# Kernel tuning notes

Measured on AMD Instinct MI355X. Metric: run time of the kernel, lower is better.

The kernel has to match this reference:

```python
import jax, jax.numpy as jnp
import numpy as np

B, S, D_MODEL = 2, 8192, 768
NUM_HEADS = 12
R = 4          # dilation_rate (= number of independent attention branches)
SEG = 512      # segment_size


def setup_inputs() -> dict:
    key = jax.random.key(0)
    ks = jax.random.split(key, 3)
    x = jax.random.normal(ks[0], (B, S, D_MODEL), jnp.float32)
    # Per-offset MHA weights: fused qkv proj and output proj (bias zeros)
    Wqkv = jax.random.normal(ks[1], (R, 3 * D_MODEL, D_MODEL), jnp.float32) * 0.02
    bqkv = jnp.zeros((R, 3 * D_MODEL), jnp.float32)
    Wout = jax.random.normal(ks[2], (R, D_MODEL, D_MODEL), jnp.float32) * 0.02
    bout = jnp.zeros((R, D_MODEL), jnp.float32)
    return {"x": x, "Wqkv": Wqkv, "bqkv": bqkv, "Wout": Wout, "bout": bout,
            "num_heads": NUM_HEADS}


def reference(x, Wqkv, bqkv, Wout, bout, num_heads):
    Bb, Ss, D = x.shape
    r = Wqkv.shape[0]
    L = Ss // r                # tokens per dilation offset
    n_seg = L // SEG           # segments per offset
    hd = D // num_heads

    # Dilated strided gather: x[:, o::r, :] for all offsets o -> (r, B, L, D)
    xo = jnp.moveaxis(x.reshape(Bb, L, r, D), 2, 0)

    # Per-offset fused qkv projection
    qkv = jnp.einsum('rbld,red->rble', xo, Wqkv) + bqkv[:, None, None, :]
    q, k, v = jnp.split(qkv, 3, axis=-1)
    seg = lambda t: t.reshape(r, Bb, n_seg, SEG, num_heads, hd)
    q, k, v = seg(q), seg(k), seg(v)  # (r, B, n_seg, SEG, H, hd)

    scale = 1.0 / np.sqrt(hd).astype(np.float32)
    scores = jnp.einsum('rbnqhd,rbnkhd->rbnhqk', q, k) * scale
    attn = jax.nn.softmax(scores, axis=-1)
    ctx = jnp.einsum('rbnhqk,rbnkhd->rbnqhd', attn, v).reshape(r, Bb, L, D)

    # Per-offset output projection
    out = jnp.einsum('rbld,red->rble', ctx, Wout) + bout[:, None, None, :]  # (r,B,L,D)

    # Scatter each offset's output back to its strided positions, zeros elsewhere,
    # then concat over offsets along the feature dim -> (B, S, r*D)
    res = jnp.zeros((Bb, Ss, r * D), x.dtype)
    for o in range(r):  # fixed small loop over dilation offsets
        res = res.at[:, o::r, o * D:(o + 1) * D].set(out[o])
    return res
```

## Files before the change

### kernel.cpp

```cpp
#include <hip/hip_runtime.h>

constexpr int Bb   = 2;
constexpr int S    = 8192;
constexpr int D    = 768;
constexpr int H    = 12;
constexpr int HD   = 64;
constexpr int R    = 4;
constexpr int L    = 2048;
constexpr int SEG  = 512;
constexpr int NSEG = 4;
constexpr int E3   = 3 * D;
constexpr int RD   = R * D;

typedef _Float16 f16x8 __attribute__((ext_vector_type(8)));
typedef _Float16 f16x4 __attribute__((ext_vector_type(4)));
typedef float    f32x4 __attribute__((ext_vector_type(4)));

#define AS1 __attribute__((address_space(1)))
#define AS3 __attribute__((address_space(3)))

__device__ __forceinline__ void gld16(const void* g, void* l) {
    __builtin_amdgcn_global_load_lds((AS1 void*)g, (AS3 void*)l, 16, 0, 0);
}

__global__ __launch_bounds__(256) void conv_one(const float4* __restrict__ x,
                                                f16x4* __restrict__ o, int n4)
{
    int i = blockIdx.x * 256 + threadIdx.x;
    const int stride = gridDim.x * 256;
    for (; i < n4; i += stride) {
        float4 v = x[i];
        f16x4 h;
        h[0] = (_Float16)v.x; h[1] = (_Float16)v.y;
        h[2] = (_Float16)v.z; h[3] = (_Float16)v.w;
        o[i] = h;
    }
}

template <int MODE>
__global__ __launch_bounds__(256) void mfma_gemm(const _Float16* __restrict__ Ah0,
                                                 const _Float16* __restrict__ Wh0,
                                                 const float* __restrict__ B0,
                                                 _Float16* __restrict__ Q0,
                                                 _Float16* __restrict__ K0,
                                                 _Float16* __restrict__ V0,
                                                 float* __restrict__ C0)
{
    constexpr int NXB = (MODE == 0) ? 18 : 6;
    constexpr int NWG = NXB * 16 * 8;
    const int wg = ((int)blockIdx.x & 7) * (NWG >> 3) + ((int)blockIdx.x >> 3);
    const int n0 = (wg % NXB) * 128;
    const int m0 = ((wg / NXB) & 15) * 128;
    const int z  = wg / (NXB * 16);
    const int r = z >> 1, b = z & 1;

    const _Float16* Ah; const _Float16* Wh; const float* bias;
    int lda;
    if (MODE == 0) {
        Ah = Ah0 + ((size_t)b * S + r) * D;  lda = RD;
        Wh = Wh0 + (size_t)r * E3 * D;
        bias = B0 + r * E3;
    } else {
        Ah = Ah0 + (size_t)z * L * D;        lda = D;
        Wh = Wh0 + (size_t)r * D * D;
        bias = B0 + r * D;
    }

    const int tid  = threadIdx.x;
    const int wave = tid >> 6;
    const int lane = tid & 63;
    const int lw   = lane & 15;
    const int quad = lane >> 4;
    const int wm   = wave & 1, wn = wave >> 1;

    __shared__ _Float16 sm[3][2][4096];

    f32x4 acc[4][4];
    #pragma unroll
    for (int mt = 0; mt < 4; mt++)
        #pragma unroll
        for (int nt = 0; nt < 4; nt++)
            acc[mt][nt] = f32x4{0.f, 0.f, 0.f, 0.f};

    const int srow = lane & 15;
    const int scol = (lane >> 4) * 8;

    auto stage = [&](int buf, int k0) {
        #pragma unroll
        for (int i = 0; i < 4; i++) {
            const int idx  = wave * 4 + i;
            const int tile = idx >> 3, g = idx & 7;
            const _Float16* src = (tile == 0) ? Ah : Wh;
            const int ldr   = (tile == 0) ? lda : D;
            const int base0 = (tile == 0) ? m0 : n0;
            gld16(src + (size_t)(base0 + g * 16 + srow) * ldr + k0 + scol,
                  &sm[buf][tile][g * 512]);
        }
    };

    stage(0, 0);
    stage(1, 32);

    for (int k = 0; k < 24; k++) {
        asm volatile("s_waitcnt lgkmcnt(0)" ::: "memory");
        if (k == 23) asm volatile("s_waitcnt vmcnt(0)" ::: "memory");
        else         asm volatile("s_waitcnt vmcnt(4)" ::: "memory");
        __builtin_amdgcn_s_barrier();
        __builtin_amdgcn_sched_barrier(0);

        const int buf = k % 3;
        f16x8 af[4], bf[4];
        #pragma unroll
        for (int mt = 0; mt < 4; mt++)
            af[mt] = *(const f16x8*)&sm[buf][0][(wm * 4 + mt) * 512 + quad * 128 + lw * 8];
        #pragma unroll
        for (int nt = 0; nt < 4; nt++)
            bf[nt] = *(const f16x8*)&sm[buf][1][(wn * 4 + nt) * 512 + quad * 128 + lw * 8];
        if (k + 2 < 24) stage((k + 2) % 3, (k + 2) * 32);
        #pragma unroll
        for (int mt = 0; mt < 4; mt++)
            #pragma unroll
            for (int nt = 0; nt < 4; nt++)
                acc[mt][nt] = __builtin_amdgcn_mfma_f32_16x16x32_f16(af[mt], bf[nt], acc[mt][nt], 0, 0, 0);
    }
    __syncthreads();

    float bv[4];
    #pragma unroll
    for (int nt = 0; nt < 4; nt++)
        bv[nt] = bias[n0 + wn * 64 + nt * 16 + lw];

    if (MODE == 0) {
        const int reg = n0 / D;
        if (reg < 2) {
            _Float16* G = (reg == 0 ? Q0 : K0) + (size_t)z * L * D;
            const int colbase = (n0 - reg * D) + wn * 64;
            _Float16* wbuf = &sm[0][0][wave * 2048];
            #pragma unroll
            for (int p = 0; p < 2; p++) {
                #pragma unroll
                for (int mtl = 0; mtl < 2; mtl++) {
                    const int mt = p * 2 + mtl;
                    #pragma unroll
                    for (int nt = 0; nt < 4; nt++)
                        #pragma unroll
                        for (int rr = 0; rr < 4; rr++)
                            wbuf[(mtl * 16 + quad * 4 + rr) * 64 + nt * 16 + lw] =
                                (_Float16)(acc[mt][nt][rr] + bv[nt]);
                }
                asm volatile("s_waitcnt lgkmcnt(0)" ::: "memory");
                #pragma unroll
                for (int j = 0; j < 4; j++) {
                    const int rl = (lane >> 3) + j * 8;
                    f16x8 v = *(const f16x8*)&wbuf[rl * 64 + (lane & 7) * 8];
                    const int l = m0 + wm * 64 + p * 32 + rl;
                    *(f16x8*)(G + (size_t)l * D + colbase + (lane & 7) * 8) = v;
                }
                asm volatile("s_waitcnt lgkmcnt(0)" ::: "memory");
            }
        } else {
            #pragma unroll
            for (int nt = 0; nt < 4; nt++) {
                const int e  = (n0 - 2 * D) + wn * 64 + nt * 16 + lw;
                const int hh = e >> 6, hd = e & 63;
                #pragma unroll
                for (int mt = 0; mt < 4; mt++) {
                    const int l = m0 + wm * 64 + mt * 16 + quad * 4;
                    const int ns = l >> 9, key = l & 511;
                    f16x4 v;
                    #pragma unroll
                    for (int rr = 0; rr < 4; rr++)
                        v[rr] = (_Float16)(acc[mt][nt][rr] + bv[nt]);
                    *(f16x4*)(V0 + ((size_t)((z * H + hh) * NSEG + ns)) * (HD * SEG)
                              + (size_t)hd * SEG + key) = v;
                }
            }
        }
    } else {
        float* Crow = C0 + (size_t)b * S * RD;
        #pragma unroll
        for (int mt = 0; mt < 4; mt++)
            #pragma unroll
            for (int nt = 0; nt < 4; nt++) {
                const int col = n0 + wn * 64 + nt * 16 + lw;
                #pragma unroll
                for (int rr = 0; rr < 4; rr++) {
                    const int l = m0 + wm * 64 + mt * 16 + quad * 4 + rr;
                    const float val = acc[mt][nt][rr] + bv[nt];
                    const size_t rowoff = (size_t)(l * R + r) * RD;
                    #pragma unroll
                    for (int rp = 0; rp < 4; rp++)
                        Crow[rowoff + rp * D + col] = (rp == r) ? val : 0.f;
                }
            }
    }
}

__global__ __launch_bounds__(256) void attn_mfma(const _Float16* __restrict__ Qh,
                                                 const _Float16* __restrict__ Kh,
                                                 const _Float16* __restrict__ Vt,
                                                 _Float16* __restrict__ ctx)
{
    __shared__ _Float16 Ks[3][4096];
    __shared__ _Float16 Vs[3][4096];
    __shared__ _Float16 Pw[16384];

    int t = ((int)blockIdx.x & 7) * 96 + ((int)blockIdx.x >> 3);
    const int qh = t & 1; t >>= 1;
    const int h  = t % H; t /= H;
    const int n  = t & 3; t >>= 2;
    const int z  = t;

    const int tid  = threadIdx.x;
    const int wave = tid >> 6;
    const int lane = tid & 63;
    const int lw   = lane & 15;
    const int quad = lane >> 4;
    const int srow = lane & 15;
    const int scol = (lane >> 4) * 8;

    const _Float16* Qg = Qh + ((size_t)(z * L + n * SEG + qh * 256)) * D + h * HD;
    #pragma unroll
    for (int i = 0; i < 8; i++) {
        const int qg = wave * 4 + (i >> 1), h2 = i & 1;
        gld16(Qg + (size_t)(qg * 16 + srow) * D + h2 * 32 + scol,
              &Pw[qg * 1024 + h2 * 512]);
    }
    __syncthreads();

    f16x8 qf[4][2];
    #pragma unroll
    for (int mt = 0; mt < 4; mt++)
        #pragma unroll
        for (int kk = 0; kk < 2; kk++)
            qf[mt][kk] = *(const f16x8*)&Pw[(wave * 4 + mt) * 1024 + (kk * 4 + quad) * 128 + lw * 8];

    const _Float16* Kg = Kh + ((size_t)(z * L + n * SEG)) * D + h * HD;
    const _Float16* Vg = Vt + ((size_t)((z * H + h) * NSEG + n)) * (HD * SEG);
    _Float16* Pv = Pw + wave * 4096;

    auto stageKV = [&](int buf, int kt) {
        #pragma unroll
        for (int i = 0; i < 4; i++) {
            const int idx = wave * 4 + i;
            const int j = idx & 7, g = j >> 1, h2 = j & 1;
            if (idx < 8)
                gld16(Kg + (size_t)(kt * 64 + g * 16 + srow) * D + h2 * 32 + scol,
                      &Ks[buf][g * 1024 + h2 * 512]);
            else
                gld16(Vg + (size_t)(g * 16 + srow) * SEG + kt * 64 + h2 * 32 + scol,
                      &Vs[buf][g * 1024 + h2 * 512]);
        }
    };

    f32x4 cacc[4][4];
    #pragma unroll
    for (int mt = 0; mt < 4; mt++)
        #pragma unroll
        for (int nt = 0; nt < 4; nt++)
            cacc[mt][nt] = f32x4{0.f, 0.f, 0.f, 0.f};
    float psum[4] = {0.f, 0.f, 0.f, 0.f};

    stageKV(0, 0);
    stageKV(1, 1);

    for (int kt = 0; kt < 8; kt++) {
        asm volatile("s_waitcnt lgkmcnt(0)" ::: "memory");
        if (kt == 7) asm volatile("s_waitcnt vmcnt(0)" ::: "memory");
        else         asm volatile("s_waitcnt vmcnt(4)" ::: "memory");
        __builtin_amdgcn_s_barrier();
        __builtin_amdgcn_sched_barrier(0);

        const int buf = kt % 3;
        if (kt + 2 < 8) stageKV((kt + 2) % 3, kt + 2);

        f32x4 Sc[4][4];
        #pragma unroll
        for (int mt = 0; mt < 4; mt++)
            #pragma unroll
            for (int nt = 0; nt < 4; nt++)
                Sc[mt][nt] = f32x4{0.f, 0.f, 0.f, 0.f};
        #pragma unroll
        for (int kk = 0; kk < 2; kk++)
            #pragma unroll
            for (int nt = 0; nt < 4; nt++) {
                f16x8 kf = *(const f16x8*)&Ks[buf][nt * 1024 + (kk * 4 + quad) * 128 + lw * 8];
                #pragma unroll
                for (int mt = 0; mt < 4; mt++)
                    Sc[mt][nt] = __builtin_amdgcn_mfma_f32_16x16x32_f16(kf, qf[mt][kk], Sc[mt][nt], 0, 0, 0);
            }

        #pragma unroll
        for (int mt = 0; mt < 4; mt++)
            #pragma unroll
            for (int nt = 0; nt < 4; nt++) {
                f16x4 p4;
                #pragma unroll
                for (int rr = 0; rr < 4; rr++)
                    p4[rr] = (_Float16)__expf(Sc[mt][nt][rr] * 0.125f);
                *(f16x4*)&Pv[mt * 1024 + (nt * 2 + (quad >> 1)) * 128 + lw * 8 + (quad & 1) * 4] = p4;
            }
        asm volatile("s_waitcnt lgkmcnt(0)" ::: "memory");

        #pragma unroll
        for (int kk = 0; kk < 2; kk++) {
            f16x8 pf[4], vf[4];
            #pragma unroll
            for (int mt = 0; mt < 4; mt++) {
                pf[mt] = *(const f16x8*)&Pv[mt * 1024 + (kk * 4 + quad) * 128 + lw * 8];
                float s = 0.f;
                #pragma unroll
                for (int j = 0; j < 8; j++) s += (float)pf[mt][j];
                psum[mt] += s;
            }
            #pragma unroll
            for (int nt = 0; nt < 4; nt++)
                vf[nt] = *(const f16x8*)&Vs[buf][nt * 1024 + (kk * 4 + quad) * 128 + lw * 8];
            #pragma unroll
            for (int mt = 0; mt < 4; mt++)
                #pragma unroll
                for (int nt = 0; nt < 4; nt++)
                    cacc[mt][nt] = __builtin_amdgcn_mfma_f32_16x16x32_f16(pf[mt], vf[nt], cacc[mt][nt], 0, 0, 0);
        }
    }

    #pragma unroll
    for (int mt = 0; mt < 4; mt++) {
        psum[mt] += __shfl_xor(psum[mt], 16);
        psum[mt] += __shfl_xor(psum[mt], 32);
    }
    _Float16* Cg = ctx + ((size_t)(z * L + n * SEG + qh * 256 + wave * 64)) * D + h * HD;
    #pragma unroll
    for (int mt = 0; mt < 4; mt++)
        #pragma unroll
        for (int rr = 0; rr < 4; rr++) {
            float iv = 1.0f / __shfl(psum[mt], quad * 4 + rr);
            int q = mt * 16 + quad * 4 + rr;
            #pragma unroll
            for (int nt = 0; nt < 4; nt++)
                Cg[(size_t)q * D + nt * 16 + lw] = (_Float16)(cacc[mt][nt][rr] * iv);
        }
}

extern "C" void kernel_launch(void* const* d_in, const int* in_sizes, int n_in,
                              void* d_out, int out_size, void* d_ws, size_t ws_size,
                              hipStream_t stream)
{
    const float* x    = (const float*)d_in[0];
    const float* Wqkv = (const float*)d_in[1];
    const float* bqkv = (const float*)d_in[2];
    const float* Wout = (const float*)d_in[3];
    const float* bout = (const float*)d_in[4];

    float* out = (float*)d_out;

    constexpr size_t NX   = (size_t)Bb * S * D;
    constexpr size_t NWQ  = (size_t)R * E3 * D;
    constexpr size_t NWO  = (size_t)R * D * D;
    constexpr size_t NTOK = (size_t)R * Bb * L;

    _Float16* Xh  = (_Float16*)d_ws;
    _Float16* Wqh = Xh  + NX;
    _Float16* Wo  = Wqh + NWQ;
    _Float16* Qh  = Wo  + NWO;
    _Float16* Kh  = Qh  + NTOK * D;
    _Float16* Vt  = Kh  + NTOK * D;
    _Float16* ctx = Vt  + NTOK * D;

    conv_one<<<2048, 256, 0, stream>>>((const float4*)x, (f16x4*)Xh, (int)(NX / 4));
    conv_one<<<2048, 256, 0, stream>>>((const float4*)Wqkv, (f16x4*)Wqh, (int)(NWQ / 4));
    conv_one<<<1024, 256, 0, stream>>>((const float4*)Wout, (f16x4*)Wo, (int)(NWO / 4));

    mfma_gemm<0><<<E3 / 128 * (L / 128) * R * Bb, 256, 0, stream>>>(
        Xh, Wqh, bqkv, Qh, Kh, Vt, nullptr);

    attn_mfma<<<R * Bb * NSEG * H * 2, 256, 0, stream>>>(Qh, Kh, Vt, ctx);

    mfma_gemm<1><<<D / 128 * (L / 128) * R * Bb, 256, 0, stream>>>(
        ctx, Wo, bout, nullptr, nullptr, nullptr, out);
}
```

Baseline: 465.6 us.

## Enlarge GEMM tiles to 256x128, fold softmax scale into Q, use MFMA row sums

Both projection GEMMs now use 512-thread blocks computing 256x128 output tiles, with eight waves arranged 4x2, so each staged weight tile is reused across twice as many rows. The softmax scale times log2(e) is folded into Q at the QKV epilogue, so attention can call exp2f directly without a multiply. Per-row softmax denominators are now accumulated by an MFMA against a ones vector, replacing the scalar fp16 summation and the cross-lane shuffles. Risks are lower occupancy from larger blocks, extra MFMA work for the sums, and fp16 precision loss from pre-scaling Q.

```diff
diff --git a/kernel.cpp b/kernel.cpp
--- a/kernel.cpp
+++ b/kernel.cpp
@@ -38,7 +38,7 @@
 }
 
 template <int MODE>
-__global__ __launch_bounds__(256) void mfma_gemm(const _Float16* __restrict__ Ah0,
+__global__ __launch_bounds__(512) void mfma_gemm(const _Float16* __restrict__ Ah0,
                                                  const _Float16* __restrict__ Wh0,
                                                  const float* __restrict__ B0,
                                                  _Float16* __restrict__ Q0,
@@ -47,11 +47,12 @@
                                                  float* __restrict__ C0)
 {
     constexpr int NXB = (MODE == 0) ? 18 : 6;
-    constexpr int NWG = NXB * 16 * 8;
+    constexpr int MB  = 8;
+    constexpr int NWG = NXB * MB * 8;
     const int wg = ((int)blockIdx.x & 7) * (NWG >> 3) + ((int)blockIdx.x >> 3);
     const int n0 = (wg % NXB) * 128;
-    const int m0 = ((wg / NXB) & 15) * 128;
-    const int z  = wg / (NXB * 16);
+    const int m0 = ((wg / NXB) & (MB - 1)) * 256;
+    const int z  = wg / (NXB * MB);
     const int r = z >> 1, b = z & 1;
 
     const _Float16* Ah; const _Float16* Wh; const float* bias;
@@ -71,9 +72,9 @@
     const int lane = tid & 63;
     const int lw   = lane & 15;
     const int quad = lane >> 4;
-    const int wm   = wave & 1, wn = wave >> 1;
-
-    __shared__ _Float16 sm[3][2][4096];
+    const int wm   = wave & 3, wn = wave >> 2;
+
+    __shared__ _Float16 sm[3][12288];
 
     f32x4 acc[4][4];
     #pragma unroll
@@ -87,14 +88,15 @@
 
     auto stage = [&](int buf, int k0) {
         #pragma unroll
-        for (int i = 0; i < 4; i++) {
-            const int idx  = wave * 4 + i;
-            const int tile = idx >> 3, g = idx & 7;
-            const _Float16* src = (tile == 0) ? Ah : Wh;
-            const int ldr   = (tile == 0) ? lda : D;
-            const int base0 = (tile == 0) ? m0 : n0;
+        for (int i = 0; i < 3; i++) {
+            const int idx  = wave * 3 + i;
+            const bool isA = idx < 16;
+            const int g    = isA ? idx : idx - 16;
+            const _Float16* src = isA ? Ah : Wh;
+            const int ldr   = isA ? lda : D;
+            const int base0 = isA ? m0 : n0;
             gld16(src + (size_t)(base0 + g * 16 + srow) * ldr + k0 + scol,
-                  &sm[buf][tile][g * 512]);
+                  &sm[buf][(isA ? 0 : 8192) + g * 512]);
         }
     };
 
@@ -104,7 +106,7 @@
     for (int k = 0; k < 24; k++) {
         asm volatile("s_waitcnt lgkmcnt(0)" ::: "memory");
         if (k == 23) asm volatile("s_waitcnt vmcnt(0)" ::: "memory");
-        else         asm volatile("s_waitcnt vmcnt(4)" ::: "memory");
+        else         asm volatile("s_waitcnt vmcnt(3)" ::: "memory");
         __builtin_amdgcn_s_barrier();
         __builtin_amdgcn_sched_barrier(0);
 
@@ -112,10 +114,10 @@
         f16x8 af[4], bf[4];
         #pragma unroll
         for (int mt = 0; mt < 4; mt++)
-            af[mt] = *(const f16x8*)&sm[buf][0][(wm * 4 + mt) * 512 + quad * 128 + lw * 8];
+            af[mt] = *(const f16x8*)&sm[buf][(wm * 4 + mt) * 512 + quad * 128 + lw * 8];
         #pragma unroll
         for (int nt = 0; nt < 4; nt++)
-            bf[nt] = *(const f16x8*)&sm[buf][1][(wn * 4 + nt) * 512 + quad * 128 + lw * 8];
+            bf[nt] = *(const f16x8*)&sm[buf][8192 + (wn * 4 + nt) * 512 + quad * 128 + lw * 8];
         if (k + 2 < 24) stage((k + 2) % 3, (k + 2) * 32);
         #pragma unroll
         for (int mt = 0; mt < 4; mt++)
@@ -133,9 +135,10 @@
     if (MODE == 0) {
         const int reg = n0 / D;
         if (reg < 2) {
+            const float qs = (reg == 0) ? 0.18033688011112042f : 1.0f;
             _Float16* G = (reg == 0 ? Q0 : K0) + (size_t)z * L * D;
             const int colbase = (n0 - reg * D) + wn * 64;
-            _Float16* wbuf = &sm[0][0][wave * 2048];
+            _Float16* wbuf = &sm[0][wave * 2048];
             #pragma unroll
             for (int p = 0; p < 2; p++) {
                 #pragma unroll
@@ -146,7 +149,7 @@
                         #pragma unroll
                         for (int rr = 0; rr < 4; rr++)
                             wbuf[(mtl * 16 + quad * 4 + rr) * 64 + nt * 16 + lw] =
-                                (_Float16)(acc[mt][nt][rr] + bv[nt]);
+                                (_Float16)((acc[mt][nt][rr] + bv[nt]) * qs);
                 }
                 asm volatile("s_waitcnt lgkmcnt(0)" ::: "memory");
                 #pragma unroll
@@ -259,7 +262,13 @@
         #pragma unroll
         for (int nt = 0; nt < 4; nt++)
             cacc[mt][nt] = f32x4{0.f, 0.f, 0.f, 0.f};
-    float psum[4] = {0.f, 0.f, 0.f, 0.f};
+    f32x4 Ps[4];
+    #pragma unroll
+    for (int mt = 0; mt < 4; mt++)
+        Ps[mt] = f32x4{0.f, 0.f, 0.f, 0.f};
+    f16x8 ones;
+    #pragma unroll
+    for (int j = 0; j < 8; j++) ones[j] = (_Float16)1.0f;
 
     stageKV(0, 0);
     stageKV(1, 1);
@@ -297,7 +306,7 @@
                 f16x4 p4;
                 #pragma unroll
                 for (int rr = 0; rr < 4; rr++)
-                    p4[rr] = (_Float16)__expf(Sc[mt][nt][rr] * 0.125f);
+                    p4[rr] = (_Float16)exp2f(Sc[mt][nt][rr]);
                 *(f16x4*)&Pv[mt * 1024 + (nt * 2 + (quad >> 1)) * 128 + lw * 8 + (quad & 1) * 4] = p4;
             }
         asm volatile("s_waitcnt lgkmcnt(0)" ::: "memory");
@@ -306,35 +315,27 @@
         for (int kk = 0; kk < 2; kk++) {
             f16x8 pf[4], vf[4];
             #pragma unroll
-            for (int mt = 0; mt < 4; mt++) {
+            for (int mt = 0; mt < 4; mt++)
                 pf[mt] = *(const f16x8*)&Pv[mt * 1024 + (kk * 4 + quad) * 128 + lw * 8];
-                float s = 0.f;
-                #pragma unroll
-                for (int j = 0; j < 8; j++) s += (float)pf[mt][j];
-                psum[mt] += s;
-            }
             #pragma unroll
             for (int nt = 0; nt < 4; nt++)
                 vf[nt] = *(const f16x8*)&Vs[buf][nt * 1024 + (kk * 4 + quad) * 128 + lw * 8];
             #pragma unroll
-            for (int mt = 0; mt < 4; mt++)
+            for (int mt = 0; mt < 4; mt++) {
+                Ps[mt] = __builtin_amdgcn_mfma_f32_16x16x32_f16(pf[mt], ones, Ps[mt], 0, 0, 0);
                 #pragma unroll
                 for (int nt = 0; nt < 4; nt++)
                     cacc[mt][nt] = __builtin_amdgcn_mfma_f32_16x16x32_f16(pf[mt], vf[nt], cacc[mt][nt], 0, 0, 0);
-        }
-    }
-
-    #pragma unroll
-    for (int mt = 0; mt < 4; mt++) {
-        psum[mt] += __shfl_xor(psum[mt], 16);
-        psum[mt] += __shfl_xor(psum[mt], 32);
-    }
+            }
+        }
+    }
+
     _Float16* Cg = ctx + ((size_t)(z * L + n * SEG + qh * 256 + wave * 64)) * D + h * HD;
     #pragma unroll
     for (int mt = 0; mt < 4; mt++)
         #pragma unroll
         for (int rr = 0; rr < 4; rr++) {
-            float iv = 1.0f / __shfl(psum[mt], quad * 4 + rr);
+            float iv = 1.0f / Ps[mt][rr];
             int q = mt * 16 + quad * 4 + rr;
             #pragma unroll
             for (int nt = 0; nt < 4; nt++)
@@ -371,11 +372,11 @@
     conv_one<<<2048, 256, 0, stream>>>((const float4*)Wqkv, (f16x4*)Wqh, (int)(NWQ / 4));
     conv_one<<<1024, 256, 0, stream>>>((const float4*)Wout, (f16x4*)Wo, (int)(NWO / 4));
 
-    mfma_gemm<0><<<E3 / 128 * (L / 128) * R * Bb, 256, 0, stream>>>(
+    mfma_gemm<0><<<E3 / 128 * (L / 256) * R * Bb, 512, 0, stream>>>(
         Xh, Wqh, bqkv, Qh, Kh, Vt, nullptr);
 
     attn_mfma<<<R * Bb * NSEG * H * 2, 256, 0, stream>>>(Qh, Kh, Vt, ctx);
 
-    mfma_gemm<1><<<D / 128 * (L / 128) * R * Bb, 256, 0, stream>>>(
+    mfma_gemm<1><<<D / 128 * (L / 256) * R * Bb, 512, 0, stream>>>(
         ctx, Wo, bout, nullptr, nullptr, nullptr, out);
 }
```

After: 492.7 us. +5.8%, slower.
